# Kernel optimization log

Measured on AMD Instinct MI355X. Metric: run time of the kernel, lower is better.

Reference implementation:

```python
import jax, jax.numpy as jnp
import numpy as np

RES_W, RES_H = 256, 256
MAX_SAMPLES = 384
TF_RES = 128
FOV_DEG = 30.0
NEAR, FAR = 0.1, 100.0
BG = 0.0
HIT_EPS = 1e-3


def _normalize(v, axis=-1):
    return v / jnp.linalg.norm(v, axis=axis, keepdims=True)


def trilinear_sample(vol, tex):
    # vol: [X,Y,Z], tex: [...,3] in voxel coordinates
    res = np.array(vol.shape, dtype=np.float32)
    p = jnp.clip(tex, 0.0, jnp.asarray(res - 1.0 - 1e-6, jnp.float32))
    lo = jnp.floor(p).astype(jnp.int32)
    f = p - lo.astype(p.dtype)
    hi = jnp.minimum(lo + 1, jnp.asarray(res.astype(np.int32) - 1))
    x0, y0, z0 = lo[..., 0], lo[..., 1], lo[..., 2]
    x1, y1, z1 = hi[..., 0], hi[..., 1], hi[..., 2]
    fx, fy, fz = f[..., 0], f[..., 1], f[..., 2]
    c000 = vol[x0, y0, z0]; c100 = vol[x1, y0, z0]
    c010 = vol[x0, y1, z0]; c110 = vol[x1, y1, z0]
    c001 = vol[x0, y0, z1]; c101 = vol[x1, y0, z1]
    c011 = vol[x0, y1, z1]; c111 = vol[x1, y1, z1]
    c00 = c000 * (1 - fx) + c100 * fx
    c10 = c010 * (1 - fx) + c110 * fx
    c01 = c001 * (1 - fx) + c101 * fx
    c11 = c011 * (1 - fx) + c111 * fx
    c0 = c00 * (1 - fy) + c10 * fy
    c1 = c01 * (1 - fy) + c11 * fy
    return c0 * (1 - fz) + c1 * fz


def tf_lookup(tf, x):
    # tf: [T,4], x: [...] intensity in [0,1]
    T = tf.shape[0]
    xi = jnp.clip(x, 0.0, 1.0) * (T - 1)
    lo = jnp.floor(xi).astype(jnp.int32)
    hi = jnp.minimum(lo + 1, T - 1)
    f = (xi - lo.astype(xi.dtype))[..., None]
    return tf[lo] * (1 - f) + tf[hi] * f


def render_one(vol, tf, cam, sr):
    # vol [X,Y,Z], tf [T,4], cam [3] -> [W,H,5] (rgba + depth)
    W, H = RES_W, RES_H
    fwd = _normalize(-cam)
    world_up = jnp.array([0.0, 1.0, 0.0], jnp.float32)
    right = _normalize(jnp.cross(fwd, world_up))
    up = jnp.cross(right, fwd)
    tanf = jnp.tan(jnp.float32(np.radians(FOV_DEG) / 2))
    aspect = W / H
    u = ((jnp.arange(W) + 0.5) / W * 2 - 1) * tanf * aspect  # [W]
    v = ((jnp.arange(H) + 0.5) / H * 2 - 1) * tanf           # [H]
    dirs = fwd + u[:, None, None] * right + v[None, :, None] * up  # [W,H,3]
    dirs = _normalize(dirs)
    # ray-box intersection against [-1,1]^3
    inv = 1.0 / dirs
    t_lo = (-1.0 - cam) * inv
    t_hi = (1.0 - cam) * inv
    tmin = jnp.max(jnp.minimum(t_lo, t_hi), axis=-1)
    tmax = jnp.min(jnp.maximum(t_lo, t_hi), axis=-1)
    hit = (tmax >= 0.0) & (tmin <= tmax)
    entry = jnp.maximum(tmin, NEAR)
    dist = jnp.where(hit, jnp.maximum(tmax - entry, 0.0), 0.0)
    vol_max = max(vol.shape)
    # Nyquist: step = voxel size (2/vol_max) / sampling_rate
    ns = jnp.clip(jnp.ceil(dist * 0.5 * vol_max * sr), 1.0, MAX_SAMPLES)
    step = dist / ns
    k = jnp.arange(MAX_SAMPLES, dtype=jnp.float32)
    t = entry[..., None] + (k + 0.5) * step[..., None]            # [W,H,S]
    valid = (k < ns[..., None]) & hit[..., None]
    pos = cam + t[..., None] * dirs[..., None, :]                 # [W,H,S,3]
    res_m1 = jnp.asarray(np.array(vol.shape, np.float32) - 1.0)
    tex = (pos * 0.5 + 0.5) * res_m1
    intensity = trilinear_sample(vol, tex)                        # [W,H,S]
    rgba = tf_lookup(tf, intensity)                               # [W,H,S,4]
    a = rgba[..., 3]
    a = 1.0 - (1.0 - a) ** (1.0 / sr)   # opacity correction for sampling rate
    a = jnp.where(valid, a, 0.0)
    one_m = 1.0 - a
    cp = jnp.cumprod(one_m, axis=-1)
    T_excl = jnp.concatenate([jnp.ones_like(cp[..., :1]), cp[..., :-1]], axis=-1)
    w = T_excl * a                                                # [W,H,S]
    rgb = jnp.einsum('whs,whsc->whc', w, rgba[..., :3])
    acc = jnp.sum(w, axis=-1)
    rgb_out = rgb + (1.0 - acc)[..., None] * BG
    # FirstHitDepth
    hit_s = a > HIT_EPS
    any_hit = jnp.any(hit_s, axis=-1)
    first = jnp.argmax(hit_s, axis=-1)
    t_first = jnp.take_along_axis(t, first[..., None], axis=-1)[..., 0]
    depth = jnp.where(any_hit, (t_first - NEAR) / (FAR - NEAR), 1.0)
    return jnp.concatenate([rgb_out, acc[..., None], depth[..., None]], axis=-1)


def setup_inputs() -> dict:
    key = jax.random.key(0)
    k1, k2, k3 = jax.random.split(key, 3)
    volume = jax.random.uniform(k1, (1, 256, 256, 256), dtype=jnp.float32)
    tf = jax.random.uniform(k2, (1, TF_RES, 4), dtype=jnp.float32)
    look_from = jnp.array([[0.9, 0.7, -2.2]], jnp.float32) + 0.1 * jax.random.normal(k3, (1, 3), dtype=jnp.float32)
    return {"volume": volume, "tf": tf, "look_from": look_from, "sampling_rate": 1}


def reference(volume, tf, look_from, sampling_rate):
    sr = float(sampling_rate)
    return jax.vmap(lambda v, t, c: render_one(v, t, c, sr))(volume, tf, look_from)
```

## Files before the change

kernel.cpp:

```cpp
#include <hip/hip_runtime.h>
#include <math.h>

#define RES_W 256
#define RES_H 256
#define MAX_SAMPLES 384
#define TF_RES 128

__global__ __launch_bounds__(64) void raycast_kernel(
    const float* __restrict__ vol,
    const float* __restrict__ tf,
    const float* __restrict__ cam_p,
    const int*   __restrict__ sr_p,
    float* __restrict__ out)
{
    #pragma clang fp contract(off)

    __shared__ float4 tf_s[TF_RES];
    const int tid = (int)threadIdx.x;
    const float4* tf4 = (const float4*)tf;
    tf_s[tid]      = tf4[tid];
    tf_s[tid + 64] = tf4[tid + 64];
    __syncthreads();

    const int b    = (int)blockIdx.x;
    const int tile = (b % 8) * 128 + (b / 8);
    const int tile_h = tile % 32;
    const int tile_w = tile / 32;
    const int h = tile_h * 8 + (tid % 8);
    const int w = tile_w * 8 + (tid / 8);

    const float cx = cam_p[0], cy = cam_p[1], cz = cam_p[2];
    const int   sr_i = sr_p[0];
    const float srf = (float)sr_i;

    float nx = -cx, ny = -cy, nz = -cz;
    float fl = __fsqrt_rn((nx*nx + ny*ny) + nz*nz);
    float fx = nx / fl, fy = ny / fl, fz = nz / fl;
    float rxu = 0.0f - fz;
    float rzu = fx;
    float rl = __fsqrt_rn((rxu*rxu + 0.0f) + rzu*rzu);
    float rx = rxu / rl, rz = rzu / rl;
    float ux = 0.0f - rz*fy;
    float uy = rz*fx - rx*fz;
    float uz = rx*fy;

    const float ang32 = (float)((30.0 * 0.017453292519943295) * 0.5);
    const float tan_half = (float)tan((double)ang32);

    float uu = ((((float)w + 0.5f) / 256.0f) * 2.0f - 1.0f) * tan_half;
    float vv = ((((float)h + 0.5f) / 256.0f) * 2.0f - 1.0f) * tan_half;

    float dx = (fx + uu*rx) + vv*ux;
    float dy = (fy + 0.0f ) + vv*uy;
    float dz = (fz + uu*rz) + vv*uz;
    float dl = __fsqrt_rn((dx*dx + dy*dy) + dz*dz);
    dx = dx / dl; dy = dy / dl; dz = dz / dl;

    float ivx = 1.0f/dx, ivy = 1.0f/dy, ivz = 1.0f/dz;
    float tlx = (-1.0f - cx)*ivx, thx = (1.0f - cx)*ivx;
    float tly = (-1.0f - cy)*ivy, thy = (1.0f - cy)*ivy;
    float tlz = (-1.0f - cz)*ivz, thz = (1.0f - cz)*ivz;
    float tmin = fmaxf(fmaxf(fminf(tlx,thx), fminf(tly,thy)), fminf(tlz,thz));
    float tmax = fminf(fminf(fmaxf(tlx,thx), fmaxf(tly,thy)), fmaxf(tlz,thz));
    bool hit = (tmax >= 0.0f) && (tmin <= tmax);

    float entry = fmaxf(tmin, 0.1f);
    float dist  = hit ? fmaxf(tmax - entry, 0.0f) : 0.0f;
    float nsf   = fminf(fmaxf(ceilf(((dist * 0.5f) * 256.0f) * srf), 1.0f), 384.0f);
    int   ns    = (int)nsf;
    float step  = dist / nsf;

    float rgb_r = 0.0f, rgb_g = 0.0f, rgb_b = 0.0f;
    float acc = 0.0f;
    float Texcl = 1.0f;
    float depth = 1.0f;
    bool  found = false;

    if (hit) {
        for (int k0 = 0; k0 < ns; k0 += 4) {
            float t_[4], val[4][8], ffx_[4], ffy_[4], ffz_[4];
            #pragma unroll
            for (int j = 0; j < 4; ++j) {
                float t  = entry + ((float)(k0 + j) + 0.5f) * step;
                t_[j] = t;
                float px = (cx + t*dx);
                float py = (cy + t*dy);
                float pz = (cz + t*dz);
                px = ((px * 0.5f) + 0.5f) * 255.0f;
                py = ((py * 0.5f) + 0.5f) * 255.0f;
                pz = ((pz * 0.5f) + 0.5f) * 255.0f;
                px = fminf(fmaxf(px, 0.0f), 255.0f);
                py = fminf(fmaxf(py, 0.0f), 255.0f);
                pz = fminf(fmaxf(pz, 0.0f), 255.0f);
                int x0 = (int)floorf(px), y0 = (int)floorf(py), z0 = (int)floorf(pz);
                ffx_[j] = px - (float)x0;
                ffy_[j] = py - (float)y0;
                ffz_[j] = pz - (float)z0;
                int x1 = min(x0 + 1, 255);
                int y1 = min(y0 + 1, 255);
                int z1 = min(z0 + 1, 255);
                int bx0 = x0 << 16, bx1 = x1 << 16;
                int by0 = y0 << 8,  by1 = y1 << 8;
                val[j][0] = vol[bx0 + by0 + z0];
                val[j][1] = vol[bx1 + by0 + z0];
                val[j][2] = vol[bx0 + by1 + z0];
                val[j][3] = vol[bx1 + by1 + z0];
                val[j][4] = vol[bx0 + by0 + z1];
                val[j][5] = vol[bx1 + by0 + z1];
                val[j][6] = vol[bx0 + by1 + z1];
                val[j][7] = vol[bx1 + by1 + z1];
            }
            float tfr_[4];
            float4 ca_[4], cb_[4];
            #pragma unroll
            for (int j = 0; j < 4; ++j) {
                float omx = 1.0f - ffx_[j], omy = 1.0f - ffy_[j], omz = 1.0f - ffz_[j];
                float c00 = val[j][0]*omx + val[j][1]*ffx_[j];
                float c10 = val[j][2]*omx + val[j][3]*ffx_[j];
                float c01 = val[j][4]*omx + val[j][5]*ffx_[j];
                float c11 = val[j][6]*omx + val[j][7]*ffx_[j];
                float c0  = c00*omy + c10*ffy_[j];
                float c1  = c01*omy + c11*ffy_[j];
                float intensity = c0*omz + c1*ffz_[j];
                float xi = fminf(fmaxf(intensity, 0.0f), 1.0f) * 127.0f;
                int lo  = (int)floorf(xi);
                int hi2 = min(lo + 1, 127);
                tfr_[j] = xi - (float)lo;
                ca_[j] = tf_s[lo];
                cb_[j] = tf_s[hi2];
            }
            #pragma unroll
            for (int j = 0; j < 4; ++j) {
                if (k0 + j < ns) {
                    float tfr = tfr_[j];
                    float omt = 1.0f - tfr;
                    float cr  = ca_[j].x*omt + cb_[j].x*tfr;
                    float cg  = ca_[j].y*omt + cb_[j].y*tfr;
                    float cbb = ca_[j].z*omt + cb_[j].z*tfr;
                    float a   = ca_[j].w*omt + cb_[j].w*tfr;
                    if (sr_i == 1) {
                        a = 1.0f - (1.0f - a);
                    } else {
                        a = 1.0f - powf(1.0f - a, 1.0f / srf);
                    }
                    float one_m = 1.0f - a;
                    float wgt = Texcl * a;
                    rgb_r += wgt * cr;
                    rgb_g += wgt * cg;
                    rgb_b += wgt * cbb;
                    acc   += wgt;
                    if (!found && a > 1e-3f) {
                        found = true;
                        depth = (t_[j] - 0.1f) / 99.9f;
                    }
                    Texcl = Texcl * one_m;
                }
            }
            if (found && Texcl < 1e-7f) break;
        }
    }

    {
        int oi = (w * RES_H + h) * 5;
        out[oi + 0] = rgb_r;
        out[oi + 1] = rgb_g;
        out[oi + 2] = rgb_b;
        out[oi + 3] = acc;
        out[oi + 4] = depth;
    }
}

extern "C" void kernel_launch(void* const* d_in, const int* in_sizes, int n_in,
                              void* d_out, int out_size, void* d_ws, size_t ws_size,
                              hipStream_t stream) {
    const float* vol = (const float*)d_in[0];
    const float* tf  = (const float*)d_in[1];
    const float* cam = (const float*)d_in[2];
    const int*   sr  = (const int*)d_in[3];
    float* out = (float*)d_out;

    raycast_kernel<<<dim3(1024), dim3(64), 0, stream>>>(vol, tf, cam, sr, out);
}
```

Measured before the change: 113.0 us.

## Split each ray into four sample segments across waves and composite in LDS

Each block now runs 256 threads, with four wavefronts each marching a 96-sample segment of the same 64 rays. Partial colour, alpha, transmittance and first-hit depth go to shared memory, and the first wave composites them front to back. This raises parallelism and occupancy, since 1024 blocks of 64 threads underfill the GPU and serial ray marching limits latency hiding. In exchange it gives up early ray termination across segments, because later segments march even when earlier ones are opaque. It also reduces the unroll from 4 to 2 and changes the float summation order, which may shift results slightly.

```diff
diff --git a/kernel.cpp b/kernel.cpp
--- a/kernel.cpp
+++ b/kernel.cpp
@@ -5,8 +5,10 @@
 #define RES_H 256
 #define MAX_SAMPLES 384
 #define TF_RES 128
-
-__global__ __launch_bounds__(64) void raycast_kernel(
+#define NSEG 4
+#define SEG_LEN 96
+
+__global__ __launch_bounds__(256, 4) void raycast_kernel(
     const float* __restrict__ vol,
     const float* __restrict__ tf,
     const float* __restrict__ cam_p,
@@ -16,18 +18,22 @@
     #pragma clang fp contract(off)
 
     __shared__ float4 tf_s[TF_RES];
-    const int tid = (int)threadIdx.x;
-    const float4* tf4 = (const float4*)tf;
-    tf_s[tid]      = tf4[tid];
-    tf_s[tid + 64] = tf4[tid + 64];
-    __syncthreads();
+    __shared__ float seg_r[NSEG][64], seg_g[NSEG][64], seg_b[NSEG][64];
+    __shared__ float seg_a[NSEG][64], seg_T[NSEG][64], seg_d[NSEG][64];
+    __shared__ int   seg_f[NSEG][64];
+
+    const int tid  = (int)threadIdx.x;
+    const int lane = tid & 63;
+    const int seg  = tid >> 6;
+
+    if (tid < TF_RES) tf_s[tid] = ((const float4*)tf)[tid];
 
     const int b    = (int)blockIdx.x;
     const int tile = (b % 8) * 128 + (b / 8);
     const int tile_h = tile % 32;
     const int tile_w = tile / 32;
-    const int h = tile_h * 8 + (tid % 8);
-    const int w = tile_w * 8 + (tid / 8);
+    const int h = tile_h * 8 + (lane % 8);
+    const int w = tile_w * 8 + (lane / 8);
 
     const float cx = cam_p[0], cy = cam_p[1], cz = cam_p[2];
     const int   sr_i = sr_p[0];
@@ -70,17 +76,22 @@
     int   ns    = (int)nsf;
     float step  = dist / nsf;
 
+    __syncthreads();
+
     float rgb_r = 0.0f, rgb_g = 0.0f, rgb_b = 0.0f;
     float acc = 0.0f;
     float Texcl = 1.0f;
     float depth = 1.0f;
     bool  found = false;
 
-    if (hit) {
-        for (int k0 = 0; k0 < ns; k0 += 4) {
-            float t_[4], val[4][8], ffx_[4], ffy_[4], ffz_[4];
+    const int k_begin = seg * SEG_LEN;
+    const int k_end   = min(ns, (seg + 1) * SEG_LEN);
+
+    if (hit && k_begin < k_end) {
+        for (int k0 = k_begin; k0 < k_end; k0 += 2) {
+            float t_[2], val[2][8], ffx_[2], ffy_[2], ffz_[2];
             #pragma unroll
-            for (int j = 0; j < 4; ++j) {
+            for (int j = 0; j < 2; ++j) {
                 float t  = entry + ((float)(k0 + j) + 0.5f) * step;
                 t_[j] = t;
                 float px = (cx + t*dx);
@@ -110,10 +121,10 @@
                 val[j][6] = vol[bx0 + by1 + z1];
                 val[j][7] = vol[bx1 + by1 + z1];
             }
-            float tfr_[4];
-            float4 ca_[4], cb_[4];
+            float tfr_[2];
+            float4 ca_[2], cb_[2];
             #pragma unroll
-            for (int j = 0; j < 4; ++j) {
+            for (int j = 0; j < 2; ++j) {
                 float omx = 1.0f - ffx_[j], omy = 1.0f - ffy_[j], omz = 1.0f - ffz_[j];
                 float c00 = val[j][0]*omx + val[j][1]*ffx_[j];
                 float c10 = val[j][2]*omx + val[j][3]*ffx_[j];
@@ -130,8 +141,8 @@
                 cb_[j] = tf_s[hi2];
             }
             #pragma unroll
-            for (int j = 0; j < 4; ++j) {
-                if (k0 + j < ns) {
+            for (int j = 0; j < 2; ++j) {
+                if (k0 + j < k_end) {
                     float tfr = tfr_[j];
                     float omt = 1.0f - tfr;
                     float cr  = ca_[j].x*omt + cb_[j].x*tfr;
@@ -160,13 +171,33 @@
         }
     }
 
-    {
+    seg_r[seg][lane] = rgb_r;
+    seg_g[seg][lane] = rgb_g;
+    seg_b[seg][lane] = rgb_b;
+    seg_a[seg][lane] = acc;
+    seg_T[seg][lane] = Texcl;
+    seg_d[seg][lane] = depth;
+    seg_f[seg][lane] = found ? 1 : 0;
+    __syncthreads();
+
+    if (tid < 64) {
+        float T = 1.0f, r = 0.0f, g = 0.0f, bb = 0.0f, ac = 0.0f, dp = 1.0f;
+        bool fnd = false;
+        #pragma unroll
+        for (int s = 0; s < NSEG; ++s) {
+            r  += T * seg_r[s][tid];
+            g  += T * seg_g[s][tid];
+            bb += T * seg_b[s][tid];
+            ac += T * seg_a[s][tid];
+            if (!fnd && seg_f[s][tid]) { fnd = true; dp = seg_d[s][tid]; }
+            T = T * seg_T[s][tid];
+        }
         int oi = (w * RES_H + h) * 5;
-        out[oi + 0] = rgb_r;
-        out[oi + 1] = rgb_g;
-        out[oi + 2] = rgb_b;
-        out[oi + 3] = acc;
-        out[oi + 4] = depth;
+        out[oi + 0] = r;
+        out[oi + 1] = g;
+        out[oi + 2] = bb;
+        out[oi + 3] = ac;
+        out[oi + 4] = dp;
     }
 }
 
@@ -179,5 +210,5 @@
     const int*   sr  = (const int*)d_in[3];
     float* out = (float*)d_out;
 
-    raycast_kernel<<<dim3(1024), dim3(64), 0, stream>>>(vol, tf, cam, sr, out);
+    raycast_kernel<<<dim3(1024), dim3(256), 0, stream>>>(vol, tf, cam, sr, out);
 }
```

New measurement: 154.5 us. 36.7% more time.
